# Optimization experiments

Measured on AMD Instinct MI355X. Metric: run time of the kernel, lower is better.

The kernel has to match this reference:

```python
import jax, jax.numpy as jnp
import numpy as np

# --- KAN_Convolution (b_spline) constants per init_kwargs ---
K = 3                      # kernel side
IN_F = K * K               # KANLinear in_features = prod(kernel_size)
GRID_SIZE = 5
SPLINE_ORDER = 3
GRID_LO, GRID_HI = -1.0, 1.0
STRIDE = (1, 1)
PAD = (1, 1)
DIL = (1, 1)


def make_grid():
    # efficient-kan grid: extended by spline_order knots on each side
    h = (GRID_HI - GRID_LO) / GRID_SIZE
    g = jnp.arange(-SPLINE_ORDER, GRID_SIZE + SPLINE_ORDER + 1, dtype=jnp.float32) * h + GRID_LO
    return jnp.broadcast_to(g, (IN_F, g.shape[0]))  # (in, G) with G = grid_size + 2*order + 1


def b_splines(x, grid):
    # x: (M, in) -> (M, in, grid_size + spline_order) via Cox-de-Boor recursion
    x = x[..., None]  # (M, in, 1)
    bases = ((x >= grid[:, :-1]) & (x < grid[:, 1:])).astype(x.dtype)
    for k in range(1, SPLINE_ORDER + 1):
        left = (x - grid[:, : -(k + 1)]) / (grid[:, k:-1] - grid[:, : -(k + 1)])
        right = (grid[:, k + 1 :] - x) / (grid[:, k + 1 :] - grid[:, 1:-k])
        bases = left * bases[..., :-1] + right * bases[..., 1:]
    return bases


def setup_inputs() -> dict:
    key = jax.random.key(0)
    k1, k2, k3, k4 = jax.random.split(key, 4)
    B, C, H, W = 8, 32, 64, 64
    x = jax.random.normal(k1, (B, C, H, W), jnp.float32)
    # KANLinear(in_features=9, out_features=1) parameters
    base_weight = jax.random.normal(k2, (1, IN_F), jnp.float32) * 0.3
    spline_weight = jax.random.normal(k3, (1, IN_F, GRID_SIZE + SPLINE_ORDER), jnp.float32) * 0.1
    spline_scaler = jax.random.normal(k4, (1, IN_F), jnp.float32) * 0.3 + 1.0
    return {
        "x": x,
        "base_weight": base_weight,
        "spline_weight": spline_weight,
        "spline_scaler": spline_scaler,
    }


def reference(x, base_weight, spline_weight, spline_scaler):
    B, C, H, W = x.shape
    # kan_conv2d: unfold each channel independently into (k*k)-patches,
    # then apply the shared KANLinear to every patch.
    patches = jax.lax.conv_general_dilated_patches(
        x.reshape(B * C, 1, H, W),
        filter_shape=(K, K),
        window_strides=STRIDE,
        padding=[(PAD[0], PAD[0]), (PAD[1], PAD[1])],
        rhs_dilation=DIL,
    )  # (B*C, K*K, Ho, Wo); feature order = row-major (kh, kw) like torch Unfold
    _, F, Ho, Wo = patches.shape
    p = jnp.transpose(patches, (0, 2, 3, 1)).reshape(-1, F)  # (M, 9)

    grid = make_grid()
    # base path: SiLU then linear (use_linear=True, base_activation=SiLU)
    base = jnp.dot(jax.nn.silu(p), base_weight.T)  # (M, 1)
    # spline path: B-spline bases contracted with scaled spline weights
    scaled_w = spline_weight * spline_scaler[..., None]  # (out, in, coef)
    sp = jnp.einsum("mic,oic->mo", b_splines(p, grid), scaled_w)  # (M, 1)

    out = (base + sp).reshape(B * C, Ho, Wo).reshape(B, C, Ho, Wo)
    return out
```

## Files before the change

### kernel.cpp

```cpp
#include <hip/hip_runtime.h>
#include <hip/hip_bf16.h>


constexpr int HW    = 64;
constexpr int PLANE = HW * HW;
constexpr int NPIX  = 8 * 32 * PLANE;

__global__ __launch_bounds__(256) void kan_conv(
    const float* __restrict__ x,
    const float* __restrict__ bw,
    const float* __restrict__ sw,
    const float* __restrict__ sc,
    float* __restrict__ out)
{
    __shared__ float s_bw[9];
    __shared__ float s_sw[9][14];

    const int t = threadIdx.x;
    if (t < 9 * 14) {
        const int i = t / 14, q = t % 14;
        float v = 0.f;
        if (q >= 3 && q <= 10)
            v = sw[i * 8 + (q - 3)] * sc[i];
        s_sw[i][q] = v;
    }
    if (t < 9) s_bw[t] = bw[t];
    __syncthreads();

    const int idx = blockIdx.x * 256 + t;
    const int rem = idx & (PLANE - 1);
    const int h   = rem >> 6;
    const int w   = rem & (HW - 1);
    const float* __restrict__ xp = x + (size_t)(idx >> 12) * PLANE;

    float acc = 0.f;
    #pragma unroll
    for (int kh = 0; kh < 3; ++kh) {
        const int  ih = h + kh - 1;
        const bool hv = (unsigned)ih < (unsigned)HW;
        #pragma unroll
        for (int kw = 0; kw < 3; ++kw) {
            const int  iw    = w + kw - 1;
            const bool valid = hv && ((unsigned)iw < (unsigned)HW);
            const float v = valid ? xp[ih * HW + iw] : 0.f;
            const int   i = kh * 3 + kw;

            const float sig = 1.f / (1.f + __expf(-v));
            acc += s_bw[i] * v * sig;

            const float s  = (v + 2.2f) * 2.5f;
            const float fm = floorf(s);
            int   m0 = (int)fm;
            const float u  = s - fm;
            const bool  inr = (m0 >= 0) && (m0 <= 10);
            m0 = inr ? m0 : 0;
            const float mul = inr ? (1.f / 6.f) : 0.f;
            const float u2 = u * u, u3 = u2 * u;
            const float om = 1.f - u;
            const float w0 = om * om * om * mul;
            const float w1 = (3.f * u3 - 6.f * u2 + 4.f) * mul;
            const float w2 = (-3.f * u3 + 3.f * u2 + 3.f * u + 1.f) * mul;
            const float w3 = u3 * mul;
            const float* __restrict__ wi = s_sw[i];
            acc += wi[m0] * w0 + wi[m0 + 1] * w1 + wi[m0 + 2] * w2 + wi[m0 + 3] * w3;
        }
    }
    out[idx] = acc;
}

extern "C" void kernel_launch(void* const* d_in, const int* in_sizes, int n_in,
                              void* d_out, int out_size, void* d_ws, size_t ws_size,
                              hipStream_t stream) {
    const float* x  = (const float*)d_in[0];
    const float* bw = (const float*)d_in[1];
    const float* sw = (const float*)d_in[2];
    const float* sc = (const float*)d_in[3];
    float* o = (float*)d_out;

    const int npix = NPIX;
    kan_conv<<<npix / 256, 256, 0, stream>>>(x, bw, sw, sc, o);
}
```

Before: 75.86 us.

## Precompute per-pixel spline features in shared-memory halo tiles with polynomial coefficient tables

Each block now handles a 16x16 output tile of one plane. Every input pixel of the 18x18 halo is loaded once, and its SiLU value, fractional offset and interval index are computed once and stored in shared memory. Before, each pixel's sigmoid and basis work was redone nine times, once per neighbouring output. The spline weights are also folded into per-interval cubic polynomial coefficients, so each tap becomes a float4 lookup plus a few FMAs. The cost is extra shared memory, a larger halo load and a different tile-based output indexing.

```diff
diff --git a/kernel.cpp b/kernel.cpp
--- a/kernel.cpp
+++ b/kernel.cpp
@@ -1,10 +1,11 @@
 #include <hip/hip_runtime.h>
-#include <hip/hip_bf16.h>
 
 
 constexpr int HW    = 64;
 constexpr int PLANE = HW * HW;
-constexpr int NPIX  = 8 * 32 * PLANE;
+constexpr int TILE  = 16;
+constexpr int HT    = TILE + 2;
+constexpr int NF    = HT * HT;
 
 __global__ __launch_bounds__(256) void kan_conv(
     const float* __restrict__ x,
@@ -13,59 +14,77 @@
     const float* __restrict__ sc,
     float* __restrict__ out)
 {
-    __shared__ float s_bw[9];
-    __shared__ float s_sw[9][14];
+    __shared__ float4 s_f[NF];
+    __shared__ float4 s_c[12 * 9];
+    __shared__ float  s_bw[9];
 
-    const int t = threadIdx.x;
-    if (t < 9 * 14) {
-        const int i = t / 14, q = t % 14;
-        float v = 0.f;
-        if (q >= 3 && q <= 10)
-            v = sw[i * 8 + (q - 3)] * sc[i];
-        s_sw[i][q] = v;
+    const int t     = threadIdx.x;
+    const int bid   = blockIdx.x;
+    const int plane = bid >> 4;
+    const int tile  = bid & 15;
+    const int th0   = (tile >> 2) * TILE;
+    const int tw0   = (tile & 3) * TILE;
+    const float* __restrict__ xp = x + (size_t)plane * PLANE;
+
+    if (t < 108) {
+        const int i = t / 12, m = t % 12;
+        float4 c = {0.f, 0.f, 0.f, 0.f};
+        if (m < 11) {
+            const float sci = sc[i];
+            float W[4];
+            #pragma unroll
+            for (int k = 0; k < 4; ++k) {
+                const int q = m + k;
+                W[k] = (q >= 3 && q <= 10) ? sw[i * 8 + q - 3] * sci : 0.f;
+            }
+            c.x = (W[0] + 4.f * W[1] + W[2]) * (1.f / 6.f);
+            c.y = (W[2] - W[0]) * 0.5f;
+            c.z = (W[0] - 2.f * W[1] + W[2]) * 0.5f;
+            c.w = (W[3] - W[0]) * (1.f / 6.f) + (W[1] - W[2]) * 0.5f;
+        }
+        s_c[m * 9 + i] = c;
     }
     if (t < 9) s_bw[t] = bw[t];
+
+    for (int p = t; p < NF; p += 256) {
+        const int pr = p / HT, pc = p % HT;
+        const int gh = th0 - 1 + pr, gw = tw0 - 1 + pc;
+        const bool valid = ((unsigned)gh < (unsigned)HW) && ((unsigned)gw < (unsigned)HW);
+        const float v = valid ? xp[gh * HW + gw] : 0.f;
+
+        const float sig = 1.f / (1.f + __expf(-v));
+        const float s   = (v + 2.2f) * 2.5f;
+        const float fm  = floorf(s);
+        const int   m0  = (int)fm;
+        const float u   = s - fm;
+        const int   m0c = ((unsigned)m0 <= 10u) ? m0 : 11;
+
+        float4 f;
+        f.x = v * sig;
+        f.y = u;
+        f.z = u * u;
+        f.w = __int_as_float(m0c * (9 * 16));
+        s_f[p] = f;
+    }
     __syncthreads();
 
-    const int idx = blockIdx.x * 256 + t;
-    const int rem = idx & (PLANE - 1);
-    const int h   = rem >> 6;
-    const int w   = rem & (HW - 1);
-    const float* __restrict__ xp = x + (size_t)(idx >> 12) * PLANE;
-
+    const int tx = t & 15, ty = t >> 4;
+    const float4* __restrict__ fb = &s_f[ty * HT + tx];
     float acc = 0.f;
     #pragma unroll
     for (int kh = 0; kh < 3; ++kh) {
-        const int  ih = h + kh - 1;
-        const bool hv = (unsigned)ih < (unsigned)HW;
         #pragma unroll
         for (int kw = 0; kw < 3; ++kw) {
-            const int  iw    = w + kw - 1;
-            const bool valid = hv && ((unsigned)iw < (unsigned)HW);
-            const float v = valid ? xp[ih * HW + iw] : 0.f;
-            const int   i = kh * 3 + kw;
-
-            const float sig = 1.f / (1.f + __expf(-v));
-            acc += s_bw[i] * v * sig;
-
-            const float s  = (v + 2.2f) * 2.5f;
-            const float fm = floorf(s);
-            int   m0 = (int)fm;
-            const float u  = s - fm;
-            const bool  inr = (m0 >= 0) && (m0 <= 10);
-            m0 = inr ? m0 : 0;
-            const float mul = inr ? (1.f / 6.f) : 0.f;
-            const float u2 = u * u, u3 = u2 * u;
-            const float om = 1.f - u;
-            const float w0 = om * om * om * mul;
-            const float w1 = (3.f * u3 - 6.f * u2 + 4.f) * mul;
-            const float w2 = (-3.f * u3 + 3.f * u2 + 3.f * u + 1.f) * mul;
-            const float w3 = u3 * mul;
-            const float* __restrict__ wi = s_sw[i];
-            acc += wi[m0] * w0 + wi[m0 + 1] * w1 + wi[m0 + 2] * w2 + wi[m0 + 3] * w3;
+            const int i = kh * 3 + kw;
+            const float4 f = fb[kh * HT + kw];
+            const char* cb = (const char*)s_c + __float_as_int(f.w);
+            const float4 c = *(const float4*)(cb + i * 16);
+            const float u3  = f.y * f.z;
+            const float spl = fmaf(c.w, u3, fmaf(c.z, f.z, fmaf(c.y, f.y, c.x)));
+            acc += fmaf(s_bw[i], f.x, spl);
         }
     }
-    out[idx] = acc;
+    out[(size_t)plane * PLANE + (th0 + ty) * HW + (tw0 + tx)] = acc;
 }
 
 extern "C" void kernel_launch(void* const* d_in, const int* in_sizes, int n_in,
@@ -77,6 +96,5 @@
     const float* sc = (const float*)d_in[3];
     float* o = (float*)d_out;
 
-    const int npix = NPIX;
-    kan_conv<<<npix / 256, 256, 0, stream>>>(x, bw, sw, sc, o);
+    kan_conv<<<4096, 256, 0, stream>>>(x, bw, sw, sc, o);
 }
```

After: 67.41 us. 11.1% less time.
